# Kernel tuning notes

Measured on AMD Instinct MI355X. Metric: run time of the kernel, lower is better.

Reference implementation:

```python
import jax, jax.numpy as jnp
import numpy as np

B, C_IN, T, N, KS, C_OUT = 8, 64, 12, 4096, 3, 64


def setup_inputs() -> dict:
    key = jax.random.key(0)
    k1, k2, k3, k4 = jax.random.split(key, 4)
    x = jax.random.normal(k1, (B, C_IN, T, N), dtype=jnp.float32)
    # scale basis down so polynomial contraction stays well-conditioned
    graph_basis = jax.random.normal(k2, (KS, N, N), dtype=jnp.float32) / np.sqrt(N)
    fan_in = C_IN * KS
    bound = 1.0 / np.sqrt(fan_in)
    theta = jax.random.uniform(k3, (C_IN, C_OUT, KS), dtype=jnp.float32,
                               minval=-bound, maxval=bound)
    bias = jax.random.uniform(k4, (1, C_OUT, 1, 1), dtype=jnp.float32,
                              minval=-bound, maxval=bound)
    return {"x": x, "graph_basis": graph_basis, "theta": theta, "bias": bias}


def reference(x, graph_basis, theta, bias):
    # x: [B, c_in, T, N]; graph_basis: [ks, N, N]; theta: [c_in, c_out, ks]
    x_c = jnp.einsum('knm,bitm->bitkn', graph_basis, x)        # [B, c_in, T, ks, N]
    x_gc = jnp.einsum('iok,bitkn->botn', theta, x_c) + bias    # [B, c_out, T, N]
    # Align: c_in == c_out -> identity residual
    return jax.nn.relu(x_gc + x)
```

## Files before the change

### kernel.cpp

```cpp
#include <hip/hip_runtime.h>

#define B_    8
#define CIN   64
#define T_    12
#define N_    4096
#define KS_   3
#define COUT  64
#define P_    (B_*COUT*T_)
#define GSZ   ((size_t)N_*N_)
#define WSZ   ((size_t)P_*N_)

typedef __attribute__((ext_vector_type(8))) short bf16x8;
typedef __attribute__((ext_vector_type(4))) float f32x4;

__device__ __forceinline__ unsigned short f2bf(float f) {
  unsigned int u = __float_as_uint(f);
  u += 0x7FFF + ((u >> 16) & 1);
  return (unsigned short)(u >> 16);
}

__device__ __forceinline__ void async16(unsigned short* lds, const unsigned short* g) {
  __builtin_amdgcn_global_load_lds(
      (const __attribute__((address_space(1))) unsigned int*)g,
      (__attribute__((address_space(3))) unsigned int*)lds, 16, 0, 0);
}

__global__ __launch_bounds__(256) void cast_g(const float4* __restrict__ in,
                                              ushort4* __restrict__ out) {
  int i = blockIdx.x * 256 + threadIdx.x;
  float4 v = in[i];
  ushort4 o;
  o.x = f2bf(v.x); o.y = f2bf(v.y); o.z = f2bf(v.z); o.w = f2bf(v.w);
  out[i] = o;
}

__global__ __launch_bounds__(256) void stage1(const float* __restrict__ x,
                                              const float* __restrict__ theta,
                                              unsigned short* __restrict__ Wt) {
  __shared__ float sTh[CIN*COUT*KS_];
  for (int idx = threadIdx.x; idx < CIN*COUT*KS_; idx += 256) sTh[idx] = theta[idx];
  __syncthreads();

  int bid = blockIdx.x;
  int mc  = bid & 15;
  int bt  = bid >> 4;
  int b   = bt / T_;
  int t   = bt - b * T_;
  int m   = mc * 256 + threadIdx.x;

  const float* xp = x + ((size_t)(b * CIN) * T_ + t) * N_ + m;
  float xi[CIN];
#pragma unroll
  for (int i = 0; i < CIN; ++i) xi[i] = xp[(size_t)i * T_ * N_];

  size_t ob = ((size_t)(b * COUT) * T_ + t) * N_ + m;
  for (int o = 0; o < COUT; ++o) {
    float a0 = 0.f, a1 = 0.f, a2 = 0.f;
#pragma unroll
    for (int i = 0; i < CIN; ++i) {
      float xv = xi[i];
      a0 = fmaf(xv, sTh[(i * COUT + o) * 3 + 0], a0);
      a1 = fmaf(xv, sTh[(i * COUT + o) * 3 + 1], a1);
      a2 = fmaf(xv, sTh[(i * COUT + o) * 3 + 2], a2);
    }
    size_t pm = ob + (size_t)o * T_ * N_;
    Wt[pm]            = f2bf(a0);
    Wt[WSZ + pm]      = f2bf(a1);
    Wt[2 * WSZ + pm]  = f2bf(a2);
  }
}

#define BM 128
#define BN 128
#define BK 32

__global__ __launch_bounds__(256) void gemm_fused(const unsigned short* __restrict__ Wt,
                                                  const unsigned short* __restrict__ Gb,
                                                  const float* __restrict__ xres,
                                                  const float* __restrict__ bias,
                                                  float* __restrict__ out) {
  __shared__ unsigned short sA[BM * BK];
  __shared__ unsigned short sB[BN * BK];

  int tid = threadIdx.x;
  int l = tid & 63, w = tid >> 6;

  int bid = blockIdx.x;
  int swz = (bid & 7) * 192 + (bid >> 3);
  int pm = swz >> 5;
  int pn = swz & 31;
  int p0 = pm * BM, n0 = pn * BN;
  int wr = w >> 1, wc = w & 1;

  int srow = w * 16 + (l >> 2);
  int scol = (l & 3) * 8;
  unsigned short* ldsA0 = &sA[w * 512];
  unsigned short* ldsA1 = &sA[w * 512 + 2048];
  unsigned short* ldsB0 = &sB[w * 512];
  unsigned short* ldsB1 = &sB[w * 512 + 2048];

  f32x4 acc[4][4];
#pragma unroll
  for (int i = 0; i < 4; ++i)
#pragma unroll
    for (int j = 0; j < 4; ++j) acc[i][j] = (f32x4){0.f, 0.f, 0.f, 0.f};

  int fr = l & 15, k8 = l >> 4;

  for (int kb = 0; kb < KS_; ++kb) {
    const unsigned short* Ak = Wt + (size_t)kb * WSZ + (size_t)p0 * N_;
    const unsigned short* Bk = Gb + (size_t)kb * GSZ + (size_t)n0 * N_;
    const unsigned short* ga0 = Ak + (size_t)srow * N_ + scol;
    const unsigned short* ga1 = Ak + (size_t)(srow + 64) * N_ + scol;
    const unsigned short* gb0 = Bk + (size_t)srow * N_ + scol;
    const unsigned short* gb1 = Bk + (size_t)(srow + 64) * N_ + scol;

    for (int kt = 0; kt < N_ / BK; ++kt) {
      int ko = kt * BK;
      async16(ldsA0, ga0 + ko);
      async16(ldsA1, ga1 + ko);
      async16(ldsB0, gb0 + ko);
      async16(ldsB1, gb1 + ko);
      __syncthreads();

      bf16x8 af[4], bff[4];
#pragma unroll
      for (int mi = 0; mi < 4; ++mi)
        af[mi] = *reinterpret_cast<const bf16x8*>(&sA[(wr * 64 + mi * 16 + fr) * BK + k8 * 8]);
#pragma unroll
      for (int ni = 0; ni < 4; ++ni)
        bff[ni] = *reinterpret_cast<const bf16x8*>(&sB[(wc * 64 + ni * 16 + fr) * BK + k8 * 8]);

#pragma unroll
      for (int mi = 0; mi < 4; ++mi)
#pragma unroll
        for (int ni = 0; ni < 4; ++ni)
          acc[mi][ni] = __builtin_amdgcn_mfma_f32_16x16x32_bf16(af[mi], bff[ni], acc[mi][ni], 0, 0, 0);

      __syncthreads();
    }
  }

  int rbase = (l >> 4) * 4;
#pragma unroll
  for (int mi = 0; mi < 4; ++mi) {
#pragma unroll
    for (int ni = 0; ni < 4; ++ni) {
      f32x4 v = acc[mi][ni];
      int n = n0 + wc * 64 + ni * 16 + fr;
      int pb = p0 + wr * 64 + mi * 16 + rbase;
#pragma unroll
      for (int r = 0; r < 4; ++r) {
        int p = pb + r;
        int o = (p / T_) & (COUT - 1);
        size_t off = (size_t)p * N_ + n;
        float res = v[r] + bias[o] + xres[off];
        out[off] = fmaxf(res, 0.f);
      }
    }
  }
}

extern "C" void kernel_launch(void* const* d_in, const int* in_sizes, int n_in,
                              void* d_out, int out_size, void* d_ws, size_t ws_size,
                              hipStream_t stream) {
  const float* x     = (const float*)d_in[0];
  const float* g     = (const float*)d_in[1];
  const float* theta = (const float*)d_in[2];
  const float* bias  = (const float*)d_in[3];
  float* out = (float*)d_out;

  unsigned short* Gb = (unsigned short*)d_ws;
  unsigned short* Wt = Gb + KS_ * GSZ;

  cast_g<<<49152, 256, 0, stream>>>((const float4*)g, (ushort4*)Gb);
  stage1<<<96 * 16, 256, 0, stream>>>(x, theta, Wt);
  gemm_fused<<<1536, 256, 0, stream>>>(Wt, Gb, x, bias, out);
}
```

Before: 1.570 ms.

## Double-buffer GEMM LDS tiles, remap blocks per XCD, read theta from global

```diff
diff --git a/kernel.cpp b/kernel.cpp
--- a/kernel.cpp
+++ b/kernel.cpp
@@ -37,10 +37,6 @@
 __global__ __launch_bounds__(256) void stage1(const float* __restrict__ x,
                                               const float* __restrict__ theta,
                                               unsigned short* __restrict__ Wt) {
-  __shared__ float sTh[CIN*COUT*KS_];
-  for (int idx = threadIdx.x; idx < CIN*COUT*KS_; idx += 256) sTh[idx] = theta[idx];
-  __syncthreads();
-
   int bid = blockIdx.x;
   int mc  = bid & 15;
   int bt  = bid >> 4;
@@ -55,13 +51,14 @@
 
   size_t ob = ((size_t)(b * COUT) * T_ + t) * N_ + m;
   for (int o = 0; o < COUT; ++o) {
+    const float* tb = theta + o * KS_;
     float a0 = 0.f, a1 = 0.f, a2 = 0.f;
 #pragma unroll
     for (int i = 0; i < CIN; ++i) {
       float xv = xi[i];
-      a0 = fmaf(xv, sTh[(i * COUT + o) * 3 + 0], a0);
-      a1 = fmaf(xv, sTh[(i * COUT + o) * 3 + 1], a1);
-      a2 = fmaf(xv, sTh[(i * COUT + o) * 3 + 2], a2);
+      a0 = fmaf(xv, tb[i * COUT * KS_ + 0], a0);
+      a1 = fmaf(xv, tb[i * COUT * KS_ + 1], a1);
+      a2 = fmaf(xv, tb[i * COUT * KS_ + 2], a2);
     }
     size_t pm = ob + (size_t)o * T_ * N_;
     Wt[pm]            = f2bf(a0);
@@ -73,31 +70,29 @@
 #define BM 128
 #define BN 128
 #define BK 32
+#define NSTEP (KS_ * (N_ / BK))
 
 __global__ __launch_bounds__(256) void gemm_fused(const unsigned short* __restrict__ Wt,
                                                   const unsigned short* __restrict__ Gb,
                                                   const float* __restrict__ xres,
                                                   const float* __restrict__ bias,
                                                   float* __restrict__ out) {
-  __shared__ unsigned short sA[BM * BK];
-  __shared__ unsigned short sB[BN * BK];
+  __shared__ unsigned short sA[2][BM * BK];
+  __shared__ unsigned short sB[2][BN * BK];
 
   int tid = threadIdx.x;
   int l = tid & 63, w = tid >> 6;
 
   int bid = blockIdx.x;
-  int swz = (bid & 7) * 192 + (bid >> 3);
-  int pm = swz >> 5;
-  int pn = swz & 31;
+  int xcd = bid & 7, idx = bid >> 3;
+  int cx = xcd >> 1, cy = xcd & 1;
+  int pm = cx * 12 + idx % 12;
+  int pn = cy * 16 + idx / 12;
   int p0 = pm * BM, n0 = pn * BN;
   int wr = w >> 1, wc = w & 1;
 
   int srow = w * 16 + (l >> 2);
   int scol = (l & 3) * 8;
-  unsigned short* ldsA0 = &sA[w * 512];
-  unsigned short* ldsA1 = &sA[w * 512 + 2048];
-  unsigned short* ldsB0 = &sB[w * 512];
-  unsigned short* ldsB1 = &sB[w * 512 + 2048];
 
   f32x4 acc[4][4];
 #pragma unroll
@@ -107,38 +102,42 @@
 
   int fr = l & 15, k8 = l >> 4;
 
-  for (int kb = 0; kb < KS_; ++kb) {
-    const unsigned short* Ak = Wt + (size_t)kb * WSZ + (size_t)p0 * N_;
-    const unsigned short* Bk = Gb + (size_t)kb * GSZ + (size_t)n0 * N_;
-    const unsigned short* ga0 = Ak + (size_t)srow * N_ + scol;
-    const unsigned short* ga1 = Ak + (size_t)(srow + 64) * N_ + scol;
-    const unsigned short* gb0 = Bk + (size_t)srow * N_ + scol;
-    const unsigned short* gb1 = Bk + (size_t)(srow + 64) * N_ + scol;
+  const unsigned short* gaBase = Wt + (size_t)(p0 + srow) * N_ + scol;
+  const unsigned short* gbBase = Gb + (size_t)(n0 + srow) * N_ + scol;
 
-    for (int kt = 0; kt < N_ / BK; ++kt) {
-      int ko = kt * BK;
-      async16(ldsA0, ga0 + ko);
-      async16(ldsA1, ga1 + ko);
-      async16(ldsB0, gb0 + ko);
-      async16(ldsB1, gb1 + ko);
-      __syncthreads();
+#define STAGE(c, s)                                                                  \
+  do {                                                                               \
+    int kb_ = (s) >> 7, kt_ = (s) & 127;                                             \
+    const unsigned short* ga_ = gaBase + (size_t)kb_ * WSZ + kt_ * BK;               \
+    const unsigned short* gb_ = gbBase + (size_t)kb_ * GSZ + kt_ * BK;               \
+    async16(&sA[c][w * 512], ga_);                                                   \
+    async16(&sA[c][w * 512 + 2048], ga_ + (size_t)64 * N_);                          \
+    async16(&sB[c][w * 512], gb_);                                                   \
+    async16(&sB[c][w * 512 + 2048], gb_ + (size_t)64 * N_);                          \
+  } while (0)
 
-      bf16x8 af[4], bff[4];
+  STAGE(0, 0);
+  __syncthreads();
+
+  for (int s = 0; s < NSTEP; ++s) {
+    int cur = s & 1;
+    if (s + 1 < NSTEP) STAGE(cur ^ 1, s + 1);
+
+    bf16x8 af[4], bff[4];
 #pragma unroll
-      for (int mi = 0; mi < 4; ++mi)
-        af[mi] = *reinterpret_cast<const bf16x8*>(&sA[(wr * 64 + mi * 16 + fr) * BK + k8 * 8]);
+    for (int mi = 0; mi < 4; ++mi)
+      af[mi] = *reinterpret_cast<const bf16x8*>(&sA[cur][(wr * 64 + mi * 16 + fr) * BK + k8 * 8]);
+#pragma unroll
+    for (int ni = 0; ni < 4; ++ni)
+      bff[ni] = *reinterpret_cast<const bf16x8*>(&sB[cur][(wc * 64 + ni * 16 + fr) * BK + k8 * 8]);
+
+#pragma unroll
+    for (int mi = 0; mi < 4; ++mi)
 #pragma unroll
       for (int ni = 0; ni < 4; ++ni)
-        bff[ni] = *reinterpret_cast<const bf16x8*>(&sB[(wc * 64 + ni * 16 + fr) * BK + k8 * 8]);
+        acc[mi][ni] = __builtin_amdgcn_mfma_f32_16x16x32_bf16(af[mi], bff[ni], acc[mi][ni], 0, 0, 0);
 
-#pragma unroll
-      for (int mi = 0; mi < 4; ++mi)
-#pragma unroll
-        for (int ni = 0; ni < 4; ++ni)
-          acc[mi][ni] = __builtin_amdgcn_mfma_f32_16x16x32_bf16(af[mi], bff[ni], acc[mi][ni], 0, 0, 0);
-
-      __syncthreads();
-    }
+    __syncthreads();
   }
 
   int rbase = (l >> 4) * 4;
@@ -159,6 +158,7 @@
       }
     }
   }
+#undef STAGE
 }
 
 extern "C" void kernel_launch(void* const* d_in, const int* in_sizes, int n_in,
```

Measured after the change: 1.666 ms. 1.06x slower.
